# Kernel tuning notes

Hardware: AMD Instinct MI355X
Metric: run time of the kernel (lower is better)

## Reference

```python
import jax, jax.numpy as jnp
import numpy as np

B, N, D, H, E, K = 8, 1024, 768, 12, 4, 9
PAD = (K - 1) // 2


def _ln(x, g, b, eps=1e-5):
    m = jnp.mean(x, -1, keepdims=True)
    v = jnp.var(x, -1, keepdims=True)
    return (x - m) * jax.lax.rsqrt(v + eps) * g + b


def setup_inputs() -> dict:
    key = jax.random.key(0)
    ks = jax.random.split(key, 12)
    w = lambda k, s: jax.random.normal(k, s, jnp.float32) * 0.02
    return {
        "x": jax.random.normal(ks[0], (B, N, D), jnp.float32),
        "ff1_ln_g": jnp.ones(D), "ff1_ln_b": jnp.zeros(D),
        "ff1_w1": w(ks[1], (D, E * D)), "ff1_b1": jnp.zeros(E * D),
        "ff1_w2": w(ks[2], (E * D, D)), "ff1_b2": jnp.zeros(D),
        "attn_ln_g": jnp.ones(D), "attn_ln_b": jnp.zeros(D),
        "qkv_w": w(ks[3], (D, 3 * D)), "qkv_b": jnp.zeros(3 * D),
        "proj_w": w(ks[4], (D, D)), "proj_b": jnp.zeros(D),
        "rel_table": w(ks[5], (2 * N - 1, H)),
        "conv_ln_g": jnp.ones(D), "conv_ln_b": jnp.zeros(D),
        "pwin_w": w(ks[6], (2 * D, D)), "pwin_b": jnp.zeros(2 * D),
        "dw_w": w(ks[7], (D, 1, K)), "dw_b": jnp.zeros(D),
        "bn_g": jnp.ones(D), "bn_b": jnp.zeros(D),
        "pwout_w": w(ks[8], (D, D)), "pwout_b": jnp.zeros(D),
        "ff2_ln_g": jnp.ones(D), "ff2_ln_b": jnp.zeros(D),
        "ff2_w1": w(ks[9], (D, E * D)), "ff2_b1": jnp.zeros(E * D),
        "ff2_w2": w(ks[10], (E * D, D)), "ff2_b2": jnp.zeros(D),
        "fin_ln_g": jnp.ones(D), "fin_ln_b": jnp.zeros(D),
    }


def _ffn(x, g, b, w1, b1, w2, b2):
    h = jax.nn.gelu(_ln(x, g, b) @ w1 + b1, approximate=False)
    return h @ w2 + b2


def _attn(x, qkv_w, qkv_b, proj_w, proj_b, rel_table):
    b_, n_, c = x.shape
    hd = c // H
    qkv = (x @ qkv_w + qkv_b).reshape(b_, n_, 3, H, hd).transpose(2, 0, 3, 1, 4)
    q, k, v = qkv[0], qkv[1], qkv[2]  # (B, H, N, hd)
    scores = jnp.einsum('bhqd,bhkd->bhqk', q, k) * (hd ** -0.5)
    coords = jnp.arange(n_)
    idx = coords[None, :] - coords[:, None] + N - 1  # (N, N) in [0, 2N-2]
    bias = rel_table[idx].transpose(2, 0, 1)  # (H, N, N)
    a = jax.nn.softmax(scores + bias[None], axis=-1)
    out = jnp.einsum('bhqk,bhkd->bhqd', a, v).transpose(0, 2, 1, 3).reshape(b_, n_, c)
    return out @ proj_w + proj_b


def _conv(x, g, b, pwin_w, pwin_b, dw_w, dw_b, bn_g, bn_b, pwout_w, pwout_b):
    y = _ln(x, g, b) @ pwin_w.T + pwin_b  # pointwise-in conv as matmul -> (B, N, 2D)
    u, gate = jnp.split(y, 2, axis=-1)
    y = (u * jax.nn.sigmoid(gate)).transpose(0, 2, 1)  # GLU over channels -> (B, D, N)
    y = jax.lax.conv_general_dilated(
        y, dw_w, (1,), [(PAD, PAD)], feature_group_count=D,
        dimension_numbers=('NCH', 'OIH', 'NCH')) + dw_b[None, :, None]
    m = jnp.mean(y, (0, 2), keepdims=True)  # BatchNorm1d, training-mode batch stats
    v = jnp.var(y, (0, 2), keepdims=True)
    y = (y - m) * jax.lax.rsqrt(v + 1e-5) * bn_g[None, :, None] + bn_b[None, :, None]
    y = y * jax.nn.sigmoid(y)  # SiLU
    y = jnp.einsum('bcn,oc->bno', y, pwout_w) + pwout_b  # pointwise-out, back to (B, N, D)
    return y


def reference(x, ff1_ln_g, ff1_ln_b, ff1_w1, ff1_b1, ff1_w2, ff1_b2,
              attn_ln_g, attn_ln_b, qkv_w, qkv_b, proj_w, proj_b, rel_table,
              conv_ln_g, conv_ln_b, pwin_w, pwin_b, dw_w, dw_b, bn_g, bn_b,
              pwout_w, pwout_b, ff2_ln_g, ff2_ln_b, ff2_w1, ff2_b1, ff2_w2, ff2_b2,
              fin_ln_g, fin_ln_b):
    x = x + 0.5 * _ffn(x, ff1_ln_g, ff1_ln_b, ff1_w1, ff1_b1, ff1_w2, ff1_b2)
    x = x + _attn(_ln(x, attn_ln_g, attn_ln_b), qkv_w, qkv_b, proj_w, proj_b, rel_table)
    x = x + _conv(x, conv_ln_g, conv_ln_b, pwin_w, pwin_b, dw_w, dw_b, bn_g, bn_b, pwout_w, pwout_b)
    x = x + 0.5 * _ffn(x, ff2_ln_g, ff2_ln_b, ff2_w1, ff2_b1, ff2_w2, ff2_b2)
    return _ln(x, fin_ln_g, fin_ln_b)
```

## Files before the change

### kernel.cpp

```cpp
#include <hip/hip_runtime.h>
#include <math.h>

#define Bb 8
#define Nn 1024
#define Dd 768
#define Hh 12
#define Mm 8192

typedef __attribute__((ext_vector_type(4))) float f32x4;
typedef __attribute__((ext_vector_type(8))) __bf16 bf16x8;

__device__ __forceinline__ float bf2f(unsigned short u) {
  union { unsigned int i; float f; } v; v.i = ((unsigned int)u) << 16; return v.f;
}
__device__ __forceinline__ unsigned short f2bf(float f) {
  union { float f; unsigned int i; } v; v.f = f;
  unsigned int u = v.i;
  return (unsigned short)((u + 0x7FFFu + ((u >> 16) & 1u)) >> 16);
}
__device__ __forceinline__ unsigned int pack2bf(float a, float b) {
  union { __bf16 h[2]; unsigned int u; } x;
  x.h[0] = (__bf16)a; x.h[1] = (__bf16)b; return x.u;
}

__device__ __forceinline__ void gload16(const void* g, void* l) {
  __builtin_amdgcn_global_load_lds(
      (const __attribute__((address_space(1))) unsigned int*)g,
      (__attribute__((address_space(3))) unsigned int*)l, 16, 0, 0);
}

__device__ __forceinline__ float gelu_f(float v) {
  const float z = fabsf(v) * 0.7071067811865475f;
  const float t = __builtin_amdgcn_rcpf(1.f + 0.3275911f * z);
  const float poly = t*(0.254829592f + t*(-0.284496736f + t*(1.421413741f +
                     t*(-1.453152027f + t*1.061405429f))));
  float er = 1.f - poly * __expf(-z * z);
  er = copysignf(er, v);
  return 0.5f * v * (1.f + er);
}

template<int EPI, int NT>
__global__ __launch_bounds__(256)
void gemm_bt(const unsigned short* __restrict__ A,
             const unsigned short* __restrict__ Bt,
             const float* __restrict__ bias,
             unsigned short* __restrict__ Cbf,
             float* __restrict__ Res,
             const float* __restrict__ Xin,
             unsigned short* __restrict__ Vtr,
             int M, int N, int K, float scale)
{
  __shared__ __align__(16) unsigned short Asm[128*64];
  __shared__ __align__(16) unsigned short Bsm[NT*64];
  const int tid = threadIdx.x;
  const int wv = tid >> 6, lane = tid & 63;
  const int lr = lane & 15, lg = lane >> 4;
  const int wr = wv >> 1, wc = wv & 1;
  constexpr int JN = NT / 32;

  const int gx = gridDim.x, gy = gridDim.y;
  const int nwg = gx * gy;
  const int lin = blockIdx.y * gx + blockIdx.x;
  const int q8 = nwg >> 3, r8 = nwg & 7;
  const int xcd = lin & 7, lidx = lin >> 3;
  const int wg = ((xcd < r8) ? xcd * (q8 + 1) : r8 * (q8 + 1) + (xcd - r8) * q8) + lidx;
  const int bx = wg % gx;
  const int by = wg / gx;

  const int n0 = bx * NT, m0 = by * 128;

  f32x4 acc[4][JN] = {};

  const int srow8 = lane >> 3;
  const int scol  = ((lane & 7) ^ srow8) * 8;
  const unsigned short* Agp = A + (size_t)(m0 + wv*32 + srow8)*K + scol;
  const unsigned short* Bgp = (NT == 128)
      ? Bt + (size_t)(n0 + wv*32 + srow8)*K + scol
      : Bt + (size_t)(n0 + wv*16 + srow8)*K + scol;
  const int swr = (lr & 7) << 4;

  for (int kt = 0; kt < K; kt += 64) {
#pragma unroll
    for (int k = 0; k < 4; k++)
      gload16(Agp + (size_t)(k*8)*K + kt, Asm + (wv*32 + k*8)*64);
    if (NT == 128) {
#pragma unroll
      for (int k = 0; k < 4; k++)
        gload16(Bgp + (size_t)(k*8)*K + kt, Bsm + (wv*32 + k*8)*64);
    } else {
#pragma unroll
      for (int k = 0; k < 2; k++)
        gload16(Bgp + (size_t)(k*8)*K + kt, Bsm + (wv*16 + k*8)*64);
    }
    __syncthreads();
    bf16x8 af[4], af2[4], bfr[JN], bfr2[JN];
#pragma unroll
    for (int i = 0; i < 4; i++) {
      const char* base = (const char*)Asm + (wr*64 + i*16 + lr)*128;
      af[i]  = *(const bf16x8*)(base + ((lg*16)      ^ swr));
      af2[i] = *(const bf16x8*)(base + ((lg*16 + 64) ^ swr));
    }
#pragma unroll
    for (int j = 0; j < JN; j++) {
      const char* base = (const char*)Bsm + (wc*(NT/2) + j*16 + lr)*128;
      bfr[j]  = *(const bf16x8*)(base + ((lg*16)      ^ swr));
      bfr2[j] = *(const bf16x8*)(base + ((lg*16 + 64) ^ swr));
    }
#pragma unroll
    for (int i = 0; i < 4; i++)
#pragma unroll
      for (int j = 0; j < JN; j++) {
        acc[i][j] = __builtin_amdgcn_mfma_f32_16x16x32_bf16(af[i],  bfr[j],  acc[i][j], 0, 0, 0);
        acc[i][j] = __builtin_amdgcn_mfma_f32_16x16x32_bf16(af2[i], bfr2[j], acc[i][j], 0, 0, 0);
      }
    __syncthreads();
  }

#pragma unroll
  for (int i = 0; i < 4; i++) {
    const int rg = m0 + wr*64 + i*16 + lg*4;
    if (EPI == 3) {
#pragma unroll
      for (int j = 0; j < JN; j += 2) {
        const int cgu = n0 + wc*(NT/2) + j*16 + lr;
        const float bu = bias[cgu], bg = bias[cgu + 16];
        const int ocol = (n0 >> 1) + wc*(NT/4) + (j >> 1)*16 + lr;
#pragma unroll
        for (int e = 0; e < 4; e++) {
          float u  = acc[i][j][e]   + bu;
          float gt = acc[i][j+1][e] + bg;
          Cbf[(size_t)(rg + e) * (N >> 1) + ocol] = f2bf(u / (1.f + __expf(-gt)));
        }
      }
    } else if (EPI == 5 && n0 >= 1536) {
#pragma unroll
      for (int j = 0; j < JN; j++) {
        const int cg = n0 + wc*(NT/2) + j*16 + lr;
        const float bv = bias[cg];
        const int vo = cg - 1536;
        const int hh = vo >> 6, d = vo & 63;
        const int bb_ = rg >> 10, nn_ = rg & 1023;
        ushort4 o4;
        o4.x = f2bf(acc[i][j][0] + bv);
        o4.y = f2bf(acc[i][j][1] + bv);
        o4.z = f2bf(acc[i][j][2] + bv);
        o4.w = f2bf(acc[i][j][3] + bv);
        *(ushort4*)(Vtr + (((size_t)bb_*Hh + hh)*64 + d)*1024 + nn_) = o4;
      }
    } else {
#pragma unroll
      for (int j = 0; j < JN; j++) {
        const int cg = n0 + wc*(NT/2) + j*16 + lr;
        const float bv = bias[cg];
#pragma unroll
        for (int e = 0; e < 4; e++) {
          float v = acc[i][j][e] + bv;
          const size_t idx = (size_t)(rg + e) * N + cg;
          if (EPI == 1) {
            Cbf[idx] = f2bf(gelu_f(v));
          } else if (EPI == 0 || EPI == 5) {
            Cbf[idx] = f2bf(v);
          } else if (EPI == 2) {
            Res[idx] += scale * v;
          } else {
            Res[idx] = Xin[idx] + scale * v;
          }
        }
      }
    }
  }
}

template<bool OBF>
__global__ __launch_bounds__(256)
void ln_kernel(const float* x, const float* __restrict__ g,
               const float* __restrict__ b, void* out)
{
  const int row = blockIdx.x, tid = threadIdx.x;
  const float* xr = x + (size_t)row * Dd;
  float v0 = xr[tid], v1 = xr[tid+256], v2 = xr[tid+512];
  float s = v0+v1+v2, q = v0*v0+v1*v1+v2*v2;
  for (int off = 32; off; off >>= 1) { s += __shfl_down(s, off); q += __shfl_down(q, off); }
  __shared__ float ps[4], pq[4];
  if ((tid & 63) == 0) { ps[tid>>6] = s; pq[tid>>6] = q; }
  __syncthreads();
  s = ps[0]+ps[1]+ps[2]+ps[3]; q = pq[0]+pq[1]+pq[2]+pq[3];
  const float mean = s * (1.f/768.f);
  const float rstd = rsqrtf(q*(1.f/768.f) - mean*mean + 1e-5f);
  float y0 = (v0-mean)*rstd*g[tid]     + b[tid];
  float y1 = (v1-mean)*rstd*g[tid+256] + b[tid+256];
  float y2 = (v2-mean)*rstd*g[tid+512] + b[tid+512];
  if (OBF) {
    unsigned short* o = (unsigned short*)out + (size_t)row * Dd;
    o[tid] = f2bf(y0); o[tid+256] = f2bf(y1); o[tid+512] = f2bf(y2);
  } else {
    float* o = (float*)out + (size_t)row * Dd;
    o[tid] = y0; o[tid+256] = y1; o[tid+512] = y2;
  }
}

__global__ __launch_bounds__(256)
void prep_all(const float* __restrict__ ff1_w1, const float* __restrict__ ff1_w2,
              const float* __restrict__ qkv_w,  const float* __restrict__ proj_w,
              const float* __restrict__ ff2_w1, const float* __restrict__ ff2_w2,
              const float* __restrict__ pwin_w, const float* __restrict__ pwin_b,
              const float* __restrict__ pwout_w, const float* __restrict__ dw_w,
              unsigned short* __restrict__ wt_ff1_1, unsigned short* __restrict__ wt_ff1_2,
              unsigned short* __restrict__ wt_qkv,   unsigned short* __restrict__ wt_proj,
              unsigned short* __restrict__ wt_ff2_1, unsigned short* __restrict__ wt_ff2_2,
              unsigned short* __restrict__ wt_pwin,  float* __restrict__ bperm,
              unsigned short* __restrict__ wt_pwout, float* __restrict__ dwwT)
{
  __shared__ float t[32][33];
  const int tid = threadIdx.x;
  int bid = blockIdx.x;

  const float* src = nullptr; unsigned short* dst = nullptr;
  int K = 0, N = 0, gx = 0;
  if (bid < 2304)        { src = ff1_w1; dst = wt_ff1_1; K = 768;  N = 3072; gx = 96; }
  else if ((bid -= 2304) < 2304) { src = ff1_w2; dst = wt_ff1_2; K = 3072; N = 768;  gx = 24; }
  else if ((bid -= 2304) < 1728) { src = qkv_w;  dst = wt_qkv;   K = 768;  N = 2304; gx = 72; }
  else if ((bid -= 1728) < 576)  { src = proj_w; dst = wt_proj;  K = 768;  N = 768;  gx = 24; }
  else if ((bid -= 576)  < 2304) { src = ff2_w1; dst = wt_ff2_1; K = 768;  N = 3072; gx = 96; }
  else if ((bid -= 2304) < 2304) { src = ff2_w2; dst = wt_ff2_2; K = 3072; N = 768;  gx = 24; }
  else if ((bid -= 2304) < 1536) {
    const int r = bid;
    const int blk = r >> 7, g = (r >> 4) & 7, tt = r & 15;
    const int orig = blk*64 + ((g >> 1) << 4) + tt + ((g & 1) ? 768 : 0);
    const float* s2 = pwin_w + (size_t)orig * 768;
    unsigned short* d2 = wt_pwin + (size_t)r * 768;
    d2[tid] = f2bf(s2[tid]); d2[tid+256] = f2bf(s2[tid+256]); d2[tid+512] = f2bf(s2[tid+512]);
    if (tid == 0) bperm[r] = pwin_b[orig];
    return;
  }
  else if ((bid -= 1536) < 1024) {
    for (int i = bid*256 + tid; i < 768*768; i += 1024*256)
      wt_pwout[i] = f2bf(pwout_w[i]);
    return;
  }
  else {
    const int id = (bid - 1024)*256 + tid;
    if (id < 9*768) {
      const int k = id / 768, d = id % 768;
      dwwT[id] = dw_w[d*9 + k];
    }
    return;
  }

  const int tx = tid & 31, ty = tid >> 5;
  const int n0 = (bid % gx) * 32, k0 = (bid / gx) * 32;
#pragma unroll
  for (int i = 0; i < 4; i++) t[ty + i*8][tx] = src[(size_t)(k0 + ty + i*8)*N + n0 + tx];
  __syncthreads();
#pragma unroll
  for (int i = 0; i < 4; i++)
    dst[(size_t)(n0 + ty + i*8)*K + k0 + tx] = f2bf(t[tx][ty + i*8]);
}

__global__ __launch_bounds__(512)
void attn_kernel(const unsigned short* __restrict__ qkv,
                 const unsigned short* __restrict__ vtr,
                 const float* __restrict__ rel,
                 unsigned short* __restrict__ out)
{
  const int bh = blockIdx.x; const int b = bh / Hh, h = bh % Hh;
  const int q0 = blockIdx.y * 128;
  const int tid = threadIdx.x, wv = tid >> 6, lane = tid & 63;
  const int lr = lane & 15, lg = lane >> 4;

  __shared__ __align__(16) unsigned short Kl[64*72];
  __shared__ __align__(16) unsigned short Vt[64*72 + 64];
  __shared__ __align__(16) unsigned short Pl[8*16*72];
  __shared__ float relh[2048];

  for (int i = tid; i < 2047; i += 512) relh[i] = rel[(size_t)i*Hh + h] * 1.44269504f;

  const size_t qrow = (size_t)(b*Nn + q0 + wv*16 + lr);
  const bf16x8 qraw0 = *(const bf16x8*)(qkv + qrow*2304 + h*64 + lg*8);
  const bf16x8 qraw1 = *(const bf16x8*)(qkv + qrow*2304 + h*64 + 32 + lg*8);
  bf16x8 qf0, qf1;
#pragma unroll
  for (int e = 0; e < 8; e++) {
    qf0[e] = (__bf16)((float)qraw0[e] * 0.180336884f);
    qf1[e] = (__bf16)((float)qraw1[e] * 0.180336884f);
  }

  const int sd = tid >> 3;
  const int sc = (tid & 7) * 8;
  unsigned short* Pw = Pl + wv*16*72;

  const unsigned short* kbase = qkv + (size_t)(b*Nn + sd)*2304 + 768 + h*64 + sc;
  const unsigned short* vbase = vtr + ((size_t)bh*64 + sd)*1024 + sc;
  bf16x8 kA = *(const bf16x8*)(kbase);
  bf16x8 vA = *(const bf16x8*)(vbase);

  f32x4 O[4] = {};
  float mrow = -1e30f, lsum = 0.f;
  const int qq = q0 + wv*16 + lr;

  __syncthreads();

  for (int kt = 0; kt < Nn; kt += 64) {
    {
      *(bf16x8*)&Kl[sd*72 + sc] = kA;
      *(bf16x8*)&Vt[sd*72 + (sd>>4)*16 + sc] = vA;
    }
    __syncthreads();

    if (kt + 64 < Nn) {
      kA = *(const bf16x8*)(kbase + (size_t)(kt + 64)*2304);
      vA = *(const bf16x8*)(vbase + kt + 64);
    }

    const int bidx = kt - qq + (Nn - 1);
    f32x4 s[4];
#pragma unroll
    for (int kb = 0; kb < 4; kb++)
#pragma unroll
      for (int j = 0; j < 4; j++)
        s[kb][j] = relh[bidx + kb*16 + lg*4 + j];
#pragma unroll
    for (int kb = 0; kb < 4; kb++) {
      bf16x8 kfa = *(const bf16x8*)&Kl[(kb*16 + lr)*72 + lg*8];
      bf16x8 kfb = *(const bf16x8*)&Kl[(kb*16 + lr)*72 + 32 + lg*8];
      s[kb] = __builtin_amdgcn_mfma_f32_16x16x32_bf16(kfa, qf0, s[kb], 0, 0, 0);
      s[kb] = __builtin_amdgcn_mfma_f32_16x16x32_bf16(kfb, qf1, s[kb], 0, 0, 0);
    }

    float r = -1e30f;
#pragma unroll
    for (int kb = 0; kb < 4; kb++)
#pragma unroll
      for (int j = 0; j < 4; j++) r = fmaxf(r, s[kb][j]);
    r = fmaxf(r, __shfl_xor(r, 16)); r = fmaxf(r, __shfl_xor(r, 32));

    if (!__all(r <= mrow + 11.5f)) {
      const float mn = fmaxf(mrow, r);
      const float al = __builtin_amdgcn_exp2f(mrow - mn);
      mrow = mn;
      lsum *= al;
#pragma unroll
      for (int ni = 0; ni < 4; ni++) {
        O[ni][0]*=al; O[ni][1]*=al; O[ni][2]*=al; O[ni][3]*=al;
      }
    }

    float rs = 0.f;
    unsigned int pk[8];
#pragma unroll
    for (int kb = 0; kb < 4; kb++) {
      float p0 = __builtin_amdgcn_exp2f(s[kb][0]-mrow), p1 = __builtin_amdgcn_exp2f(s[kb][1]-mrow);
      float p2 = __builtin_amdgcn_exp2f(s[kb][2]-mrow), p3 = __builtin_amdgcn_exp2f(s[kb][3]-mrow);
      rs += (p0+p1) + (p2+p3);
      pk[kb*2]   = pack2bf(p0, p1);
      pk[kb*2+1] = pack2bf(p2, p3);
    }
    rs += __shfl_xor(rs, 16); rs += __shfl_xor(rs, 32);
    lsum += rs;

#pragma unroll
    for (int kb0 = 0; kb0 < 4; kb0++) {
      const int kb = (kb0 + lg) & 3;
      *(unsigned int*)&Pw[lr*72 + kb*16 + lg*4]     = pk[kb*2];
      *(unsigned int*)&Pw[lr*72 + kb*16 + lg*4 + 2] = pk[kb*2+1];
    }

    bf16x8 pf0 = *(const bf16x8*)&Pw[lr*72 + lg*8];
    bf16x8 pf1 = *(const bf16x8*)&Pw[lr*72 + 32 + lg*8];
#pragma unroll
    for (int dt = 0; dt < 4; dt++) {
      bf16x8 vf0 = *(const bf16x8*)&Vt[(dt*16 + lr)*72 + dt*16 + lg*8];
      bf16x8 vf1 = *(const bf16x8*)&Vt[(dt*16 + lr)*72 + dt*16 + 32 + lg*8];
      O[dt] = __builtin_amdgcn_mfma_f32_16x16x32_bf16(vf0, pf0, O[dt], 0, 0, 0);
      O[dt] = __builtin_amdgcn_mfma_f32_16x16x32_bf16(vf1, pf1, O[dt], 0, 0, 0);
    }
    __syncthreads();
  }

  const float rl = 1.f / lsum;
#pragma unroll
  for (int dt = 0; dt < 4; dt++) {
    ushort4 o4;
    o4.x = f2bf(O[dt][0]*rl); o4.y = f2bf(O[dt][1]*rl);
    o4.z = f2bf(O[dt][2]*rl); o4.w = f2bf(O[dt][3]*rl);
    *(ushort4*)(out + (size_t)(b*Nn + qq)*Dd + h*64 + dt*16 + lg*4) = o4;
  }
}

__global__ __launch_bounds__(256)
void dwconv(const unsigned short* __restrict__ glu, const float* __restrict__ dwwT,
            const float* __restrict__ dwb, unsigned short* __restrict__ z)
{
  const int id = blockIdx.x*256 + threadIdx.x;
  if (id >= (Mm/4)*96) return;
  const int t = id / 96, c8 = (id % 96) * 8;
  const int b = t / (Nn/4), n0 = (t % (Nn/4)) * 4;

  bf16x8 zero;
#pragma unroll
  for (int e = 0; e < 8; e++) zero[e] = (__bf16)0.f;

  bf16x8 g[12];
#pragma unroll
  for (int rr = 0; rr < 12; rr++) {
    const int nn = n0 + rr - 4;
    g[rr] = (nn >= 0 && nn < Nn)
        ? *(const bf16x8*)&glu[(size_t)(b*Nn + nn)*768 + c8] : zero;
  }

  float acc[4][8];
#pragma unroll
  for (int j = 0; j < 4; j++)
#pragma unroll
    for (int e = 0; e < 8; e++) acc[j][e] = dwb[c8 + e];

#pragma unroll
  for (int k = 0; k < 9; k++) {
    const float4 w0 = *(const float4*)&dwwT[k*768 + c8];
    const float4 w1 = *(const float4*)&dwwT[k*768 + c8 + 4];
    const float w[8] = {w0.x, w0.y, w0.z, w0.w, w1.x, w1.y, w1.z, w1.w};
#pragma unroll
    for (int j = 0; j < 4; j++)
#pragma unroll
      for (int e = 0; e < 8; e++)
        acc[j][e] += w[e] * (float)g[j + k][e];
  }

#pragma unroll
  for (int j = 0; j < 4; j++) {
    bf16x8 o;
#pragma unroll
    for (int e = 0; e < 8; e++) o[e] = (__bf16)acc[j][e];
    *(bf16x8*)&z[(size_t)(b*Nn + n0 + j)*768 + c8] = o;
  }
}

__global__ __launch_bounds__(192)
void bn_part(const unsigned short* __restrict__ z, float* __restrict__ psum,
             float* __restrict__ psq)
{
  const int blk = blockIdx.x, t = threadIdx.x;
  const int c4 = t * 4;
  float s0=0,s1=0,s2=0,s3=0, q0=0,q1=0,q2=0,q3=0;
  for (int r = 0; r < 128; r++) {
    ushort4 v4 = *(const ushort4*)&z[(size_t)(blk*128 + r)*Dd + c4];
    float a = bf2f(v4.x), b_ = bf2f(v4.y), c = bf2f(v4.z), d = bf2f(v4.w);
    s0 += a; s1 += b_; s2 += c; s3 += d;
    q0 += a*a; q1 += b_*b_; q2 += c*c; q3 += d*d;
  }
  float4 sv = {s0, s1, s2, s3}, qv = {q0, q1, q2, q3};
  *(float4*)&psum[(size_t)blk*Dd + c4] = sv;
  *(float4*)&psq [(size_t)blk*Dd + c4] = qv;
}

__global__ __launch_bounds__(256)
void bn_final(const float* __restrict__ psum, const float* __restrict__ psq,
              const float* __restrict__ g, const float* __restrict__ bb,
              float* __restrict__ scale, float* __restrict__ shift)
{
  const int c = blockIdx.x*256 + threadIdx.x;
  if (c >= Dd) return;
  float s = 0.f, q = 0.f;
  for (int i = 0; i < 64; i++) { s += psum[(size_t)i*Dd + c]; q += psq[(size_t)i*Dd + c]; }
  const float mean = s / (float)Mm;
  const float var  = q / (float)Mm - mean*mean;
  const float sc = g[c] * rsqrtf(var + 1e-5f);
  scale[c] = sc; shift[c] = bb[c] - mean*sc;
}

__global__ __launch_bounds__(256)
void bn_silu(const unsigned short* __restrict__ z, const float* __restrict__ scale,
             const float* __restrict__ shift, unsigned short* __restrict__ out)
{
  const int id = blockIdx.x*256 + threadIdx.x;
  if (id >= Mm*96) return;
  const int row = id / 96, c8 = (id % 96) * 8;
  bf16x8 v = *(const bf16x8*)&z[(size_t)row*Dd + c8];
  bf16x8 o;
#pragma unroll
  for (int e = 0; e < 8; e++) {
    float t = (float)v[e] * scale[c8+e] + shift[c8+e];
    o[e] = (__bf16)(t / (1.f + __expf(-t)));
  }
  *(bf16x8*)&out[(size_t)row*Dd + c8] = o;
}

extern "C" void kernel_launch(void* const* d_in, const int* in_sizes, int n_in,
                              void* d_out, int out_size, void* d_ws, size_t ws_size,
                              hipStream_t stream)
{
  const float* x        = (const float*)d_in[0];
  const float* ff1_ln_g = (const float*)d_in[1];
  const float* ff1_ln_b = (const float*)d_in[2];
  const float* ff1_w1   = (const float*)d_in[3];
  const float* ff1_b1   = (const float*)d_in[4];
  const float* ff1_w2   = (const float*)d_in[5];
  const float* ff1_b2   = (const float*)d_in[6];
  const float* attn_ln_g= (const float*)d_in[7];
  const float* attn_ln_b= (const float*)d_in[8];
  const float* qkv_w    = (const float*)d_in[9];
  const float* qkv_b    = (const float*)d_in[10];
  const float* proj_w   = (const float*)d_in[11];
  const float* proj_b   = (const float*)d_in[12];
  const float* rel_tab  = (const float*)d_in[13];
  const float* conv_ln_g= (const float*)d_in[14];
  const float* conv_ln_b= (const float*)d_in[15];
  const float* pwin_w   = (const float*)d_in[16];
  const float* pwin_b   = (const float*)d_in[17];
  const float* dw_w     = (const float*)d_in[18];
  const float* dw_b     = (const float*)d_in[19];
  const float* bn_g     = (const float*)d_in[20];
  const float* bn_b     = (const float*)d_in[21];
  const float* pwout_w  = (const float*)d_in[22];
  const float* pwout_b  = (const float*)d_in[23];
  const float* ff2_ln_g = (const float*)d_in[24];
  const float* ff2_ln_b = (const float*)d_in[25];
  const float* ff2_w1   = (const float*)d_in[26];
  const float* ff2_b1   = (const float*)d_in[27];
  const float* ff2_w2   = (const float*)d_in[28];
  const float* ff2_b2   = (const float*)d_in[29];
  const float* fin_ln_g = (const float*)d_in[30];
  const float* fin_ln_b = (const float*)d_in[31];

  char* ws = (char*)d_ws;
  size_t off = 0;
  auto alloc = [&](size_t bytes) { char* p = ws + off; off += (bytes + 255) & ~(size_t)255; return p; };
  unsigned short* wt_ff1_1 = (unsigned short*)alloc((size_t)3072*768*2);
  unsigned short* wt_ff1_2 = (unsigned short*)alloc((size_t)768*3072*2);
  unsigned short* wt_qkv   = (unsigned short*)alloc((size_t)2304*768*2);
  unsigned short* wt_proj  = (unsigned short*)alloc((size_t)768*768*2);
  unsigned short* wt_pwin  = (unsigned short*)alloc((size_t)1536*768*2);
  unsigned short* wt_pwout = (unsigned short*)alloc((size_t)768*768*2);
  unsigned short* wt_ff2_1 = (unsigned short*)alloc((size_t)3072*768*2);
  unsigned short* wt_ff2_2 = (unsigned short*)alloc((size_t)768*3072*2);
  unsigned short* ybf      = (unsigned short*)alloc((size_t)Mm*768*2);
  unsigned short* big      = (unsigned short*)alloc((size_t)Mm*3072*2);
  unsigned short* abuf     = (unsigned short*)alloc((size_t)Mm*768*2);
  float* psum    = (float*)alloc((size_t)64*768*4);
  float* psq     = (float*)alloc((size_t)64*768*4);
  float* bnscale = (float*)alloc((size_t)768*4);
  float* bnshift = (float*)alloc((size_t)768*4);
  float* dwwT    = (float*)alloc((size_t)9*768*4);
  float* bperm   = (float*)alloc((size_t)1536*4);
  if (off > ws_size) return;

  unsigned short* vtr = big + (size_t)Mm*2304;

  float* xres = (float*)d_out;
  const dim3 tb(256);

  prep_all<<<14107, tb, 0, stream>>>(ff1_w1, ff1_w2, qkv_w, proj_w, ff2_w1, ff2_w2,
                                     pwin_w, pwin_b, pwout_w, dw_w,
                                     wt_ff1_1, wt_ff1_2, wt_qkv, wt_proj,
                                     wt_ff2_1, wt_ff2_2, wt_pwin, bperm,
                                     wt_pwout, dwwT);

  ln_kernel<true><<<Mm, tb, 0, stream>>>(x, ff1_ln_g, ff1_ln_b, ybf);
  gemm_bt<1,128><<<dim3(3072/128, Mm/128), tb, 0, stream>>>(ybf, wt_ff1_1, ff1_b1, big, nullptr, nullptr, nullptr, Mm, 3072, 768, 0.f);
  gemm_bt<4,64><<<dim3(768/64, Mm/128), tb, 0, stream>>>(big, wt_ff1_2, ff1_b2, nullptr, xres, x, nullptr, Mm, 768, 3072, 0.5f);

  ln_kernel<true><<<Mm, tb, 0, stream>>>(xres, attn_ln_g, attn_ln_b, ybf);
  gemm_bt<5,128><<<dim3(2304/128, Mm/128), tb, 0, stream>>>(ybf, wt_qkv, qkv_b, big, nullptr, nullptr, vtr, Mm, 2304, 768, 0.f);
  attn_kernel<<<dim3(Bb*Hh, Nn/128), dim3(512), 0, stream>>>(big, vtr, rel_tab, abuf);
  gemm_bt<2,64><<<dim3(768/64, Mm/128), tb, 0, stream>>>(abuf, wt_proj, proj_b, nullptr, xres, nullptr, nullptr, Mm, 768, 768, 1.0f);

  ln_kernel<true><<<Mm, tb, 0, stream>>>(xres, conv_ln_g, conv_ln_b, ybf);
  gemm_bt<3,128><<<dim3(1536/128, Mm/128), tb, 0, stream>>>(ybf, wt_pwin, bperm, abuf, nullptr, nullptr, nullptr, Mm, 1536, 768, 0.f);
  dwconv<<<((Mm/4)*96)/256, tb, 0, stream>>>(abuf, dwwT, dw_b, ybf);
  bn_part<<<64, dim3(192), 0, stream>>>(ybf, psum, psq);
  bn_final<<<3, tb, 0, stream>>>(psum, psq, bn_g, bn_b, bnscale, bnshift);
  bn_silu<<<(Mm*96)/256, tb, 0, stream>>>(ybf, bnscale, bnshift, abuf);
  gemm_bt<2,64><<<dim3(768/64, Mm/128), tb, 0, stream>>>(abuf, wt_pwout, pwout_b, nullptr, xres, nullptr, nullptr, Mm, 768, 768, 1.0f);

  ln_kernel<true><<<Mm, tb, 0, stream>>>(xres, ff2_ln_g, ff2_ln_b, ybf);
  gemm_bt<1,128><<<dim3(3072/128, Mm/128), tb, 0, stream>>>(ybf, wt_ff2_1, ff2_b1, big, nullptr, nullptr, nullptr, Mm, 3072, 768, 0.f);
  gemm_bt<2,64><<<dim3(768/64, Mm/128), tb, 0, stream>>>(big, wt_ff2_2, ff2_b2, nullptr, xres, nullptr, nullptr, Mm, 768, 3072, 0.5f);

  ln_kernel<false><<<Mm, tb, 0, stream>>>(xres, fin_ln_g, fin_ln_b, (void*)xres);
}
```

Baseline: 532.4 us.

## Store residual stream in bf16 and vectorize layernorm loads

The fp32 residual stream kept in the output buffer becomes a bf16 workspace buffer. GEMM residual epilogues now read-modify-write bf16, and the layernorms read bf16 input. LayerNorm is rewritten to use 192 active threads with 4-wide vector loads and stores, and the BatchNorm partial reduction is spread over 256 blocks instead of 64. This halves residual-stream traffic and raises parallelism in the BN stats, at the cost of rounding the residual accumulator to bf16 after each sublayer, which may hurt accuracy.

```diff
diff --git a/kernel.cpp b/kernel.cpp
--- a/kernel.cpp
+++ b/kernel.cpp
@@ -45,7 +45,7 @@
              const unsigned short* __restrict__ Bt,
              const float* __restrict__ bias,
              unsigned short* __restrict__ Cbf,
-             float* __restrict__ Res,
+             unsigned short* __restrict__ Resb,
              const float* __restrict__ Xin,
              unsigned short* __restrict__ Vtr,
              int M, int N, int K, float scale)
@@ -161,9 +161,9 @@
           } else if (EPI == 0 || EPI == 5) {
             Cbf[idx] = f2bf(v);
           } else if (EPI == 2) {
-            Res[idx] += scale * v;
+            Resb[idx] = f2bf(bf2f(Resb[idx]) + scale * v);
           } else {
-            Res[idx] = Xin[idx] + scale * v;
+            Resb[idx] = f2bf(Xin[idx] + scale * v);
           }
         }
       }
@@ -171,15 +171,25 @@
   }
 }
 
-template<bool OBF>
+template<bool IBF, bool OBF>
 __global__ __launch_bounds__(256)
-void ln_kernel(const float* x, const float* __restrict__ g,
+void ln_kernel(const void* __restrict__ xin, const float* __restrict__ g,
                const float* __restrict__ b, void* out)
 {
   const int row = blockIdx.x, tid = threadIdx.x;
-  const float* xr = x + (size_t)row * Dd;
-  float v0 = xr[tid], v1 = xr[tid+256], v2 = xr[tid+512];
-  float s = v0+v1+v2, q = v0*v0+v1*v1+v2*v2;
+  const int c4 = tid * 4;
+  const bool act = tid < 192;
+  float v0 = 0.f, v1 = 0.f, v2 = 0.f, v3 = 0.f;
+  if (act) {
+    if (IBF) {
+      ushort4 u = *(const ushort4*)((const unsigned short*)xin + (size_t)row*Dd + c4);
+      v0 = bf2f(u.x); v1 = bf2f(u.y); v2 = bf2f(u.z); v3 = bf2f(u.w);
+    } else {
+      float4 f = *(const float4*)((const float*)xin + (size_t)row*Dd + c4);
+      v0 = f.x; v1 = f.y; v2 = f.z; v3 = f.w;
+    }
+  }
+  float s = v0+v1+v2+v3, q = v0*v0+v1*v1+v2*v2+v3*v3;
   for (int off = 32; off; off >>= 1) { s += __shfl_down(s, off); q += __shfl_down(q, off); }
   __shared__ float ps[4], pq[4];
   if ((tid & 63) == 0) { ps[tid>>6] = s; pq[tid>>6] = q; }
@@ -187,15 +197,20 @@
   s = ps[0]+ps[1]+ps[2]+ps[3]; q = pq[0]+pq[1]+pq[2]+pq[3];
   const float mean = s * (1.f/768.f);
   const float rstd = rsqrtf(q*(1.f/768.f) - mean*mean + 1e-5f);
-  float y0 = (v0-mean)*rstd*g[tid]     + b[tid];
-  float y1 = (v1-mean)*rstd*g[tid+256] + b[tid+256];
-  float y2 = (v2-mean)*rstd*g[tid+512] + b[tid+512];
-  if (OBF) {
-    unsigned short* o = (unsigned short*)out + (size_t)row * Dd;
-    o[tid] = f2bf(y0); o[tid+256] = f2bf(y1); o[tid+512] = f2bf(y2);
-  } else {
-    float* o = (float*)out + (size_t)row * Dd;
-    o[tid] = y0; o[tid+256] = y1; o[tid+512] = y2;
+  if (act) {
+    const float4 gg = *(const float4*)&g[c4];
+    const float4 bb4 = *(const float4*)&b[c4];
+    float y0 = (v0-mean)*rstd*gg.x + bb4.x;
+    float y1 = (v1-mean)*rstd*gg.y + bb4.y;
+    float y2 = (v2-mean)*rstd*gg.z + bb4.z;
+    float y3 = (v3-mean)*rstd*gg.w + bb4.w;
+    if (OBF) {
+      ushort4 o4 = { f2bf(y0), f2bf(y1), f2bf(y2), f2bf(y3) };
+      *(ushort4*)((unsigned short*)out + (size_t)row*Dd + c4) = o4;
+    } else {
+      float4 o4 = { y0, y1, y2, y3 };
+      *(float4*)((float*)out + (size_t)row*Dd + c4) = o4;
+    }
   }
 }
 
@@ -442,8 +457,8 @@
   const int blk = blockIdx.x, t = threadIdx.x;
   const int c4 = t * 4;
   float s0=0,s1=0,s2=0,s3=0, q0=0,q1=0,q2=0,q3=0;
-  for (int r = 0; r < 128; r++) {
-    ushort4 v4 = *(const ushort4*)&z[(size_t)(blk*128 + r)*Dd + c4];
+  for (int r = 0; r < 32; r++) {
+    ushort4 v4 = *(const ushort4*)&z[(size_t)(blk*32 + r)*Dd + c4];
     float a = bf2f(v4.x), b_ = bf2f(v4.y), c = bf2f(v4.z), d = bf2f(v4.w);
     s0 += a; s1 += b_; s2 += c; s3 += d;
     q0 += a*a; q1 += b_*b_; q2 += c*c; q3 += d*d;
@@ -461,7 +476,7 @@
   const int c = blockIdx.x*256 + threadIdx.x;
   if (c >= Dd) return;
   float s = 0.f, q = 0.f;
-  for (int i = 0; i < 64; i++) { s += psum[(size_t)i*Dd + c]; q += psq[(size_t)i*Dd + c]; }
+  for (int i = 0; i < 256; i++) { s += psum[(size_t)i*Dd + c]; q += psq[(size_t)i*Dd + c]; }
   const float mean = s / (float)Mm;
   const float var  = q / (float)Mm - mean*mean;
   const float sc = g[c] * rsqrtf(var + 1e-5f);
@@ -536,8 +551,9 @@
   unsigned short* ybf      = (unsigned short*)alloc((size_t)Mm*768*2);
   unsigned short* big      = (unsigned short*)alloc((size_t)Mm*3072*2);
   unsigned short* abuf     = (unsigned short*)alloc((size_t)Mm*768*2);
-  float* psum    = (float*)alloc((size_t)64*768*4);
-  float* psq     = (float*)alloc((size_t)64*768*4);
+  unsigned short* xbf      = (unsigned short*)alloc((size_t)Mm*768*2);
+  float* psum    = (float*)alloc((size_t)256*768*4);
+  float* psq     = (float*)alloc((size_t)256*768*4);
   float* bnscale = (float*)alloc((size_t)768*4);
   float* bnshift = (float*)alloc((size_t)768*4);
   float* dwwT    = (float*)alloc((size_t)9*768*4);
@@ -546,7 +562,6 @@
 
   unsigned short* vtr = big + (size_t)Mm*2304;
 
-  float* xres = (float*)d_out;
   const dim3 tb(256);
 
   prep_all<<<14107, tb, 0, stream>>>(ff1_w1, ff1_w2, qkv_w, proj_w, ff2_w1, ff2_w2,
@@ -555,26 +570,26 @@
                                      wt_ff2_1, wt_ff2_2, wt_pwin, bperm,
                                      wt_pwout, dwwT);
 
-  ln_kernel<true><<<Mm, tb, 0, stream>>>(x, ff1_ln_g, ff1_ln_b, ybf);
+  ln_kernel<false,true><<<Mm, tb, 0, stream>>>(x, ff1_ln_g, ff1_ln_b, ybf);
   gemm_bt<1,128><<<dim3(3072/128, Mm/128), tb, 0, stream>>>(ybf, wt_ff1_1, ff1_b1, big, nullptr, nullptr, nullptr, Mm, 3072, 768, 0.f);
-  gemm_bt<4,64><<<dim3(768/64, Mm/128), tb, 0, stream>>>(big, wt_ff1_2, ff1_b2, nullptr, xres, x, nullptr, Mm, 768, 3072, 0.5f);
-
-  ln_kernel<true><<<Mm, tb, 0, stream>>>(xres, attn_ln_g, attn_ln_b, ybf);
+  gemm_bt<4,64><<<dim3(768/64, Mm/128), tb, 0, stream>>>(big, wt_ff1_2, ff1_b2, nullptr, xbf, x, nullptr, Mm, 768, 3072, 0.5f);
+
+  ln_kernel<true,true><<<Mm, tb, 0, stream>>>(xbf, attn_ln_g, attn_ln_b, ybf);
   gemm_bt<5,128><<<dim3(2304/128, Mm/128), tb, 0, stream>>>(ybf, wt_qkv, qkv_b, big, nullptr, nullptr, vtr, Mm, 2304, 768, 0.f);
   attn_kernel<<<dim3(Bb*Hh, Nn/128), dim3(512), 0, stream>>>(big, vtr, rel_tab, abuf);
-  gemm_bt<2,64><<<dim3(768/64, Mm/128), tb, 0, stream>>>(abuf, wt_proj, proj_b, nullptr, xres, nullptr, nullptr, Mm, 768, 768, 1.0f);
-
-  ln_kernel<true><<<Mm, tb, 0, stream>>>(xres, conv_ln_g, conv_ln_b, ybf);
+  gemm_bt<2,64><<<dim3(768/64, Mm/128), tb, 0, stream>>>(abuf, wt_proj, proj_b, nullptr, xbf, nullptr, nullptr, Mm, 768, 768, 1.0f);
+
+  ln_kernel<true,true><<<Mm, tb, 0, stream>>>(xbf, conv_ln_g, conv_ln_b, ybf);
   gemm_bt<3,128><<<dim3(1536/128, Mm/128), tb, 0, stream>>>(ybf, wt_pwin, bperm, abuf, nullptr, nullptr, nullptr, Mm, 1536, 768, 0.f);
   dwconv<<<((Mm/4)*96)/256, tb, 0, stream>>>(abuf, dwwT, dw_b, ybf);
-  bn_part<<<64, dim3(192), 0, stream>>>(ybf, psum, psq);
+  bn_part<<<256, dim3(192), 0, stream>>>(ybf, psum, psq);
   bn_final<<<3, tb, 0, stream>>>(psum, psq, bn_g, bn_b, bnscale, bnshift);
   bn_silu<<<(Mm*96)/256, tb, 0, stream>>>(ybf, bnscale, bnshift, abuf);
-  gemm_bt<2,64><<<dim3(768/64, Mm/128), tb, 0, stream>>>(abuf, wt_pwout, pwout_b, nullptr, xres, nullptr, nullptr, Mm, 768, 768, 1.0f);
-
-  ln_kernel<true><<<Mm, tb, 0, stream>>>(xres, ff2_ln_g, ff2_ln_b, ybf);
+  gemm_bt<2,64><<<dim3(768/64, Mm/128), tb, 0, stream>>>(abuf, wt_pwout, pwout_b, nullptr, xbf, nullptr, nullptr, Mm, 768, 768, 1.0f);
+
+  ln_kernel<true,true><<<Mm, tb, 0, stream>>>(xbf, ff2_ln_g, ff2_ln_b, ybf);
   gemm_bt<1,128><<<dim3(3072/128, Mm/128), tb, 0, stream>>>(ybf, wt_ff2_1, ff2_b1, big, nullptr, nullptr, nullptr, Mm, 3072, 768, 0.f);
-  gemm_bt<2,64><<<dim3(768/64, Mm/128), tb, 0, stream>>>(big, wt_ff2_2, ff2_b2, nullptr, xres, nullptr, nullptr, Mm, 768, 3072, 0.5f);
-
-  ln_kernel<false><<<Mm, tb, 0, stream>>>(xres, fin_ln_g, fin_ln_b, (void*)xres);
-}
+  gemm_bt<2,64><<<dim3(768/64, Mm/128), tb, 0, stream>>>(big, wt_ff2_2, ff2_b2, nullptr, xbf, nullptr, nullptr, Mm, 768, 3072, 0.5f);
+
+  ln_kernel<true,false><<<Mm, tb, 0, stream>>>(xbf, fin_ln_g, fin_ln_b, d_out);
+}
```

Result: no change. 528.3 us (-0.8%).
